# Kernel tuning notes

Measured on AMD Instinct MI355X. Metric: run time of the kernel, lower is better.

Reference implementation:

```python
import jax, jax.numpy as jnp
import numpy as np

IN_FEATURES = 2048
OUT_FEATURES = 8192
STRIPE_SIZE = 128
NUM_STRIPES = OUT_FEATURES // STRIPE_SIZE


def setup_inputs() -> dict:
    key = jax.random.key(0)
    k_x, k_w, k_t, k_mu, k_std = jax.random.split(key, 5)
    x = jax.random.normal(k_x, (2, 256, IN_FEATURES), dtype=jnp.float32)
    weight = jax.random.normal(k_w, (IN_FEATURES, OUT_FEATURES), dtype=jnp.float32) / np.sqrt(IN_FEATURES)
    bias = jnp.zeros((OUT_FEATURES,), dtype=jnp.float32)
    thresholds = jax.random.uniform(k_t, (NUM_STRIPES, IN_FEATURES), dtype=jnp.float32)
    mu = jax.random.normal(k_mu, (IN_FEATURES,), dtype=jnp.float32)          # adj_med_computed buffer
    std = jax.random.uniform(k_std, (IN_FEATURES,), dtype=jnp.float32)       # adj_std_computed buffer
    return {"x": x, "weight": weight, "bias": bias, "thresholds": thresholds, "mu": mu, "std": std}


def reference(x, weight, bias, thresholds, mu, std):
    # Eval-mode, batch>1 path of CWICLinear.forward.
    og_shape = x.shape[:-1]
    I, O, N, S = IN_FEATURES, OUT_FEATURES, NUM_STRIPES, STRIPE_SIZE
    xc = x.reshape(-1, 1, I) - mu[None, None, :]              # (T, 1, I) centered
    thresh = (thresholds * std[None, :])[None]                # (1, N, I)
    mask = (jnp.abs(xc) > thresh).astype(x.dtype)             # (T, N, I) data-dependent sparsity
    xm = xc * mask                                            # (T, N, I)
    W = weight.T.reshape(N, S, I)                             # stripe view of weight
    y = jnp.einsum('nsi,tni->tns', W, xm).reshape(-1, O)      # stripe matmul
    post_mu = mu @ weight                                     # einsum('a b, a -> b')
    y = y + post_mu[None, :] + bias[None, :]
    flops_const = jnp.float32(I) * jnp.float32(O)
    flops_dense = jnp.zeros(og_shape, dtype=jnp.float32) + flops_const
    flops_sparse = flops_const * mask.mean(-1).mean(-1).reshape(og_shape)
    return (y.reshape(*og_shape, O), flops_dense, flops_sparse)
```

## Files before the change

### kernel.cpp

```cpp
#include <hip/hip_runtime.h>
#include <hip/hip_bf16.h>
#include <stdint.h>

#define I_DIM 2048
#define O_DIM 8192
#define T_TOK 512
#define NSTR  64
#define BK    64
#define NSTEP (I_DIM / BK)

#define TILE_B 16384

#define THR_S 16384
#define SMEM21 24576

#define WT_OFF   ((size_t)0)
#define XC_OFF   ((size_t)67108864)
#define THR_OFF  ((size_t)71303168)
#define PM_OFF   ((size_t)71827456)
#define PMB_OFF  ((size_t)73924608)
#define CNT_OFF  ((size_t)73957376)

typedef __attribute__((ext_vector_type(8))) short bf16x8;
typedef __attribute__((ext_vector_type(4))) float f32x4;
typedef __attribute__((ext_vector_type(4))) int i32x4;

__global__ __launch_bounds__(256) void cwic_prep_all(
    const float* __restrict__ w, const float* __restrict__ mu,
    const float* __restrict__ x, const float* __restrict__ thresholds,
    const float* __restrict__ stdv, char* __restrict__ wt,
    float* __restrict__ pm_part, float* __restrict__ xc,
    float* __restrict__ thrs, int* __restrict__ counts) {
  const int tid = threadIdx.x;
  __shared__ float ls[32][512];

  if (blockIdx.x >= 1024) {
    int idx = (blockIdx.x - 1024) * 256 + tid;
    float4 xv = ((const float4*)x)[idx];
    float4 mv = ((const float4*)mu)[idx & 511];
    float4 r;
    r.x = xv.x - mv.x; r.y = xv.y - mv.y; r.z = xv.z - mv.z; r.w = xv.w - mv.w;
    ((float4*)xc)[idx] = r;
    if (idx < (NSTR * I_DIM) / 4) {
      float4 t = ((const float4*)thresholds)[idx];
      float4 s = ((const float4*)stdv)[idx & 511];
      float4 ts;
      ts.x = t.x * s.x; ts.y = t.y * s.y; ts.z = t.z * s.z; ts.w = t.w * s.w;
      ((float4*)thrs)[idx] = ts;
    }
    if (idx < T_TOK) counts[idx] = 0;
    return;
  }

  const int bp = blockIdx.x;
  const int hs = bp >> 4, cc = bp & 15;
  const int step = hs >> 1, kh = hs & 1;
  const int r0 = hs * 32;
  {
    const int sr = tid >> 7, sf = tid & 127;
    #pragma unroll 4
    for (int p = 0; p < 16; ++p) {
      const int row = p * 2 + sr;
      float4 v = *(const float4*)(w + (size_t)(r0 + row) * O_DIM + cc * 512 + sf * 4);
      *(float4*)&ls[row][sf * 4] = v;
    }
  }
  __syncthreads();

  float mus[32];
  #pragma unroll
  for (int r = 0; r < 32; ++r) mus[r] = mu[r0 + r];

  #pragma unroll
  for (int ci = 0; ci < 2; ++ci) {
    const int c = tid + ci * 256;
    const int C = cc * 512 + c;
    const int n = C >> 7, o = C & 127;
    char* tb = wt + (size_t)(n * NSTEP + step) * TILE_B + (kh * 8 + (o >> 4)) * 1024;
    float pm = 0.0f;
    #pragma unroll
    for (int g = 0; g < 4; ++g) {
      unsigned hv[4];
      unsigned hprev = 0;
      #pragma unroll
      for (int e = 0; e < 8; ++e) {
        float v = ls[g * 8 + e][c];
        pm += mus[g * 8 + e] * v;
        unsigned u = __builtin_bit_cast(unsigned, v);
        unsigned r = u + 0x7fffu + ((u >> 16) & 1u);
        unsigned short h = (unsigned short)(r >> 16);
        if ((e & 1) == 0) hprev = h;
        else hv[e >> 1] = hprev | (((unsigned)h) << 16);
      }
      *(i32x4*)(tb + ((o & 15) + g * 16) * 16) = *(i32x4*)hv;
    }
    pm_part[(size_t)(step * 2 + kh) * O_DIM + C] = pm;
  }
}

__global__ void cwic_pmb(const float* __restrict__ pm_part,
                         const float* __restrict__ bias, float* __restrict__ pmb) {
  int o = blockIdx.x * 256 + threadIdx.x;
  float s = bias[o];
  #pragma unroll 8
  for (int j = 0; j < 64; ++j) s += pm_part[(size_t)j * O_DIM + o];
  pmb[o] = s;
}

__global__ __launch_bounds__(512, 4) void cwic_gemm21(
    const float* __restrict__ xc, const char* __restrict__ wt,
    const float* __restrict__ thrs, const float* __restrict__ pmb,
    float* __restrict__ y, int* __restrict__ counts) {
  extern __shared__ char smem[];
  const int b = blockIdx.x;
  const int nid = (b & 7) * 64 + (b >> 3);
  const int n = nid >> 3, tt = nid & 7;
  const int trow0 = tt * 64, ocol0 = n * 128;
  const int tid = threadIdx.x;
  const int lane = tid & 63, wid = tid >> 6;
  const int wr = wid >> 2, wc = wid & 3;
  const int l15 = lane & 15, l4 = lane >> 4;
  const int t_loc = tid >> 3, kq = tid & 7;

  float* thr_s = (float*)(smem + THR_S);
  ((float4*)thr_s)[tid] = ((const float4*)(thrs + (size_t)n * I_DIM))[tid];

  const float* xrow = xc + (size_t)(trow0 + t_loc) * I_DIM + kq * 8;
  const char* wfrag = wt + (size_t)(n * NSTEP) * TILE_B + (wc * 2) * 1024 + lane * 16;

  f32x4 acc[2][2];
  #pragma unroll
  for (int mi = 0; mi < 2; ++mi)
    #pragma unroll
    for (int ni = 0; ni < 2; ++ni) acc[mi][ni] = (f32x4)(0.0f);
  int cnt = 0;

  bf16x8 bA0, bA1, bA2, bA3, bB0, bB1, bB2, bB3;
  bA0 = *(const bf16x8*)(wfrag + 0 * 1024);
  bA1 = *(const bf16x8*)(wfrag + 1 * 1024);
  bA2 = *(const bf16x8*)(wfrag + 8 * 1024);
  bA3 = *(const bf16x8*)(wfrag + 9 * 1024);
  __syncthreads();

#define STEP21(STEP_I, CUR, B0, B1, B2, B3, NB0, NB1, NB2, NB3)                \
  {                                                                            \
    const int step_ = (STEP_I);                                                \
    const int s1_ = (step_ + 1 < NSTEP) ? step_ + 1 : step_;                   \
             \
    {                                                                          \
      const char* bp_ = wfrag + (size_t)s1_ * TILE_B;                          \
      NB0 = *(const bf16x8*)(bp_ + 0 * 1024);                                  \
      NB1 = *(const bf16x8*)(bp_ + 1 * 1024);                                  \
      NB2 = *(const bf16x8*)(bp_ + 8 * 1024);                                  \
      NB3 = *(const bf16x8*)(bp_ + 9 * 1024);                                  \
    }                                                                          \
        \
    {                                                                          \
      float4 xv0 = *(const float4*)(xrow + step_ * BK);                        \
      float4 xv1 = *(const float4*)(xrow + step_ * BK + 4);                    \
      float4 tv0 = *(const float4*)(thr_s + step_ * BK + kq * 8);              \
      float4 tv1 = *(const float4*)(thr_s + step_ * BK + kq * 8 + 4);          \
      const float xs[8] = {xv0.x, xv0.y, xv0.z, xv0.w, xv1.x, xv1.y, xv1.z, xv1.w}; \
      const float ts[8] = {tv0.x, tv0.y, tv0.z, tv0.w, tv1.x, tv1.y, tv1.z, tv1.w}; \
      bf16x8 hv8;                                                              \
      _Pragma("unroll") for (int e = 0; e < 8; ++e) {                          \
        const float xvv = xs[e], tvv = ts[e];                                  \
        bool keep = fabsf(xvv) > tvv;                                          \
        cnt += keep ? 1 : 0;                                                   \
        float a = keep ? xvv : 0.0f;                                           \
        __hip_bfloat16 h = __float2bfloat16(a);                                \
        hv8[e] = __builtin_bit_cast(short, h);                                 \
      }                                                                        \
      const int ad = t_loc * 128 + ((kq * 16) ^ ((t_loc & 7) << 4));           \
      *(bf16x8*)(smem + (CUR) + ad) = hv8;                                     \
    }                                                                          \
    __syncthreads();              \
               \
    __builtin_amdgcn_s_setprio(1);                                             \
    _Pragma("unroll") for (int s32 = 0; s32 < 2; ++s32) {                      \
      bf16x8 afh[2];                                                           \
      _Pragma("unroll") for (int mi = 0; mi < 2; ++mi) {                       \
        const int r = wr * 32 + mi * 16 + l15;                                 \
        const int ada = r * 128 + (((s32 * 64) + l4 * 16) ^ ((r & 7) << 4));   \
        afh[mi] = *(const bf16x8*)(smem + (CUR) + ada);                        \
      }                                                                        \
      bf16x8 bh0 = (s32 == 0) ? B0 : B2;                                       \
      bf16x8 bh1 = (s32 == 0) ? B1 : B3;                                       \
      _Pragma("unroll") for (int mi = 0; mi < 2; ++mi) {                       \
        acc[mi][0] = __builtin_amdgcn_mfma_f32_16x16x32_bf16(afh[mi], bh0, acc[mi][0], 0, 0, 0); \
        acc[mi][1] = __builtin_amdgcn_mfma_f32_16x16x32_bf16(afh[mi], bh1, acc[mi][1], 0, 0, 0); \
      }                                                                        \
    }                                                                          \
    __builtin_amdgcn_s_setprio(0);                                             \
     \
  }

  for (int sp = 0; sp < NSTEP; sp += 2) {
    STEP21(sp,     0,    bA0, bA1, bA2, bA3, bB0, bB1, bB2, bB3);
    STEP21(sp + 1, 8192, bB0, bB1, bB2, bB3, bA0, bA1, bA2, bA3);
  }
#undef STEP21

  cnt += __shfl_xor(cnt, 1);
  cnt += __shfl_xor(cnt, 2);
  cnt += __shfl_xor(cnt, 4);
  if (kq == 0) atomicAdd(&counts[trow0 + t_loc], cnt);

  #pragma unroll
  for (int ni = 0; ni < 2; ++ni) {
    const int o = ocol0 + wc * 32 + ni * 16 + l15;
    const float pv = pmb[o];
    #pragma unroll
    for (int mi = 0; mi < 2; ++mi) {
      const int row0 = trow0 + wr * 32 + mi * 16 + l4 * 4;
      #pragma unroll
      for (int r = 0; r < 4; ++r) {
        y[(size_t)(row0 + r) * O_DIM + o] = acc[mi][ni][r] + pv;
      }
    }
  }
}

__global__ void cwic_fin(const int* __restrict__ counts, float* __restrict__ outF) {
  int t = blockIdx.x * 256 + threadIdx.x;
  outF[t] = 16777216.0f;
  outF[T_TOK + t] = 128.0f * (float)counts[t];
}

extern "C" void kernel_launch(void* const* d_in, const int* in_sizes, int n_in,
                              void* d_out, int out_size, void* d_ws, size_t ws_size,
                              hipStream_t stream) {
  const float* x = (const float*)d_in[0];
  const float* w = (const float*)d_in[1];
  const float* bias = (const float*)d_in[2];
  const float* thresholds = (const float*)d_in[3];
  const float* mu = (const float*)d_in[4];
  const float* stdv = (const float*)d_in[5];
  float* y = (float*)d_out;

  char* ws = (char*)d_ws;
  char* wt = ws + WT_OFF;
  float* xc = (float*)(ws + XC_OFF);
  float* thrs = (float*)(ws + THR_OFF);
  float* pm_part = (float*)(ws + PM_OFF);
  float* pmb = (float*)(ws + PMB_OFF);
  int* counts = (int*)(ws + CNT_OFF);

  cwic_prep_all<<<2048, 256, 0, stream>>>(w, mu, x, thresholds, stdv, wt,
                                          pm_part, xc, thrs, counts);
  cwic_pmb<<<32, 256, 0, stream>>>(pm_part, bias, pmb);
  cwic_gemm21<<<512, 512, SMEM21, stream>>>(xc, wt, thrs, pmb, y, counts);
  cwic_fin<<<2, 256, 0, stream>>>(counts, y + (size_t)T_TOK * O_DIM);
}
```

Before: 62.43 us.

## Software-pipeline activation masking so the next tile is staged during MFMAs

```diff
diff --git a/kernel.cpp b/kernel.cpp
--- a/kernel.cpp
+++ b/kernel.cpp
@@ -12,7 +12,7 @@
 #define TILE_B 16384
 
 #define THR_S 16384
-#define SMEM21 24576
+#define SMEM22 24576
 
 #define WT_OFF   ((size_t)0)
 #define XC_OFF   ((size_t)67108864)
@@ -107,7 +107,7 @@
   pmb[o] = s;
 }
 
-__global__ __launch_bounds__(512, 4) void cwic_gemm21(
+__global__ __launch_bounds__(512, 4) void cwic_gemm22(
     const float* __restrict__ xc, const char* __restrict__ wt,
     const float* __restrict__ thrs, const float* __restrict__ pmb,
     float* __restrict__ y, int* __restrict__ counts) {
@@ -140,42 +140,46 @@
   bA1 = *(const bf16x8*)(wfrag + 1 * 1024);
   bA2 = *(const bf16x8*)(wfrag + 8 * 1024);
   bA3 = *(const bf16x8*)(wfrag + 9 * 1024);
+  float4 xp0 = *(const float4*)(xrow);
+  float4 xp1 = *(const float4*)(xrow + 4);
   __syncthreads();
 
-#define STEP21(STEP_I, CUR, B0, B1, B2, B3, NB0, NB1, NB2, NB3)                \
+  {
+    float4 tv0 = *(const float4*)(thr_s + kq * 8);
+    float4 tv1 = *(const float4*)(thr_s + kq * 8 + 4);
+    const float xs[8] = {xp0.x, xp0.y, xp0.z, xp0.w, xp1.x, xp1.y, xp1.z, xp1.w};
+    const float ts[8] = {tv0.x, tv0.y, tv0.z, tv0.w, tv1.x, tv1.y, tv1.z, tv1.w};
+    bf16x8 hv8;
+    #pragma unroll
+    for (int e = 0; e < 8; ++e) {
+      bool keep = fabsf(xs[e]) > ts[e];
+      cnt += keep ? 1 : 0;
+      float a = keep ? xs[e] : 0.0f;
+      __hip_bfloat16 h = __float2bfloat16(a);
+      hv8[e] = __builtin_bit_cast(short, h);
+    }
+    const int ad = t_loc * 128 + ((kq * 16) ^ ((t_loc & 7) << 4));
+    *(bf16x8*)(smem + 0 + ad) = hv8;
+  }
+  __syncthreads();
+
+#define STEP22(STEP_I, CUR, B0, B1, B2, B3, NB0, NB1, NB2, NB3)                \
   {                                                                            \
     const int step_ = (STEP_I);                                                \
-    const int s1_ = (step_ + 1 < NSTEP) ? step_ + 1 : step_;                   \
-             \
+    const int s1_ = step_ + 1;                                                 \
+    const int sc_ = (s1_ < NSTEP) ? s1_ : step_;                               \
+                                 \
     {                                                                          \
-      const char* bp_ = wfrag + (size_t)s1_ * TILE_B;                          \
+      const char* bp_ = wfrag + (size_t)sc_ * TILE_B;                          \
       NB0 = *(const bf16x8*)(bp_ + 0 * 1024);                                  \
       NB1 = *(const bf16x8*)(bp_ + 1 * 1024);                                  \
       NB2 = *(const bf16x8*)(bp_ + 8 * 1024);                                  \
       NB3 = *(const bf16x8*)(bp_ + 9 * 1024);                                  \
     }                                                                          \
-        \
-    {                                                                          \
-      float4 xv0 = *(const float4*)(xrow + step_ * BK);                        \
-      float4 xv1 = *(const float4*)(xrow + step_ * BK + 4);                    \
-      float4 tv0 = *(const float4*)(thr_s + step_ * BK + kq * 8);              \
-      float4 tv1 = *(const float4*)(thr_s + step_ * BK + kq * 8 + 4);          \
-      const float xs[8] = {xv0.x, xv0.y, xv0.z, xv0.w, xv1.x, xv1.y, xv1.z, xv1.w}; \
-      const float ts[8] = {tv0.x, tv0.y, tv0.z, tv0.w, tv1.x, tv1.y, tv1.z, tv1.w}; \
-      bf16x8 hv8;                                                              \
-      _Pragma("unroll") for (int e = 0; e < 8; ++e) {                          \
-        const float xvv = xs[e], tvv = ts[e];                                  \
-        bool keep = fabsf(xvv) > tvv;                                          \
-        cnt += keep ? 1 : 0;                                                   \
-        float a = keep ? xvv : 0.0f;                                           \
-        __hip_bfloat16 h = __float2bfloat16(a);                                \
-        hv8[e] = __builtin_bit_cast(short, h);                                 \
-      }                                                                        \
-      const int ad = t_loc * 128 + ((kq * 16) ^ ((t_loc & 7) << 4));           \
-      *(bf16x8*)(smem + (CUR) + ad) = hv8;                                     \
-    }                                                                          \
-    __syncthreads();              \
-               \
+                           \
+    float4 xn0 = *(const float4*)(xrow + sc_ * BK);                            \
+    float4 xn1 = *(const float4*)(xrow + sc_ * BK + 4);                        \
+          \
     __builtin_amdgcn_s_setprio(1);                                             \
     _Pragma("unroll") for (int s32 = 0; s32 < 2; ++s32) {                      \
       bf16x8 afh[2];                                                           \
@@ -192,14 +196,31 @@
       }                                                                        \
     }                                                                          \
     __builtin_amdgcn_s_setprio(0);                                             \
-     \
+              \
+    if (s1_ < NSTEP) {                                                         \
+      float4 tv0 = *(const float4*)(thr_s + s1_ * BK + kq * 8);                \
+      float4 tv1 = *(const float4*)(thr_s + s1_ * BK + kq * 8 + 4);            \
+      const float xs[8] = {xn0.x, xn0.y, xn0.z, xn0.w, xn1.x, xn1.y, xn1.z, xn1.w}; \
+      const float ts[8] = {tv0.x, tv0.y, tv0.z, tv0.w, tv1.x, tv1.y, tv1.z, tv1.w}; \
+      bf16x8 hv8;                                                              \
+      _Pragma("unroll") for (int e = 0; e < 8; ++e) {                          \
+        bool keep = fabsf(xs[e]) > ts[e];                                      \
+        cnt += keep ? 1 : 0;                                                   \
+        float a = keep ? xs[e] : 0.0f;                                         \
+        __hip_bfloat16 h = __float2bfloat16(a);                                \
+        hv8[e] = __builtin_bit_cast(short, h);                                 \
+      }                                                                        \
+      const int ad = t_loc * 128 + ((kq * 16) ^ ((t_loc & 7) << 4));           \
+      *(bf16x8*)(smem + ((CUR) ^ 8192) + ad) = hv8;                            \
+    }                                                                          \
+    __syncthreads();  \
   }
 
   for (int sp = 0; sp < NSTEP; sp += 2) {
-    STEP21(sp,     0,    bA0, bA1, bA2, bA3, bB0, bB1, bB2, bB3);
-    STEP21(sp + 1, 8192, bB0, bB1, bB2, bB3, bA0, bA1, bA2, bA3);
-  }
-#undef STEP21
+    STEP22(sp,     0,    bA0, bA1, bA2, bA3, bB0, bB1, bB2, bB3);
+    STEP22(sp + 1, 8192, bB0, bB1, bB2, bB3, bA0, bA1, bA2, bA3);
+  }
+#undef STEP22
 
   cnt += __shfl_xor(cnt, 1);
   cnt += __shfl_xor(cnt, 2);
@@ -249,6 +270,6 @@
   cwic_prep_all<<<2048, 256, 0, stream>>>(w, mu, x, thresholds, stdv, wt,
                                           pm_part, xc, thrs, counts);
   cwic_pmb<<<32, 256, 0, stream>>>(pm_part, bias, pmb);
-  cwic_gemm21<<<512, 512, SMEM21, stream>>>(xc, wt, thrs, pmb, y, counts);
+  cwic_gemm22<<<512, 512, SMEM22, stream>>>(xc, wt, thrs, pmb, y, counts);
   cwic_fin<<<2, 256, 0, stream>>>(counts, y + (size_t)T_TOK * O_DIM);
 }
```

Result: no change. 61.62 us, median of 2 (-1.3%).
